# Kernel tuning notes

Measured on AMD Instinct MI355X. Metric: run time of the kernel, lower is better.

## Reference

```python
import jax, jax.numpy as jnp
import numpy as np

N_LABELS = 2048
N_CLASSES = 2
BATCH = 2048
BRANCH = 4


def _tree():
    # deterministic rooted tree: parent(i) = (i-1)//BRANCH, node 0 is root
    parent = np.full(N_LABELS, -1, dtype=np.int64)
    parent[1:] = (np.arange(1, N_LABELS) - 1) // BRANCH
    depth = np.zeros(N_LABELS, dtype=np.int64)
    for i in range(1, N_LABELS):
        depth[i] = depth[parent[i]] + 1
    levels = [np.where(depth == d)[0] for d in range(int(depth.max()) + 1)]
    return parent, levels

_PARENT, _LEVELS = _tree()  # static structure (from the adjacency init arg)


def setup_inputs() -> dict:
    key = jax.random.key(0)
    k1, k2 = jax.random.split(key)
    emissions = jax.random.normal(k1, (BATCH, N_CLASSES, N_LABELS), dtype=jnp.float32)
    pairs = jax.random.normal(k2, (N_LABELS, N_LABELS, N_CLASSES, N_CLASSES), dtype=jnp.float32)
    return {"emissions": emissions, "pairs": pairs}


def _messages(emissions, pairs, upward):
    """Belief-propagation messages, level-synchronous (topological order).

    upward=True  -> alphas: messages from children to parents (leaves->root)
    upward=False -> betas:  messages from parents to children (root->leaves)
    """
    B, C, L = emissions.shape
    acc = jnp.zeros((B, C, L), emissions.dtype)
    if upward:
        # process deepest level first; all nodes at level d send to their
        # (level d-1) parents; duplicate parent indices accumulate via .add
        for d in range(len(_LEVELS) - 1, 0, -1):
            nodes = _LEVELS[d]      # senders (children), (K,)
            par = _PARENT[nodes]    # receivers (parents), (K,)
            # local[b, k, yc] = emissions[b, yc, node_k] + acc[b, yc, node_k]
            local = (emissions[:, :, nodes] + acc[:, :, nodes]).transpose(0, 2, 1)
            trans = pairs[par, nodes]  # (K, Cp, Cc): pairs[parent, child]
            # msg[b, k, yp] = logsumexp_yc( trans[k, yp, yc] + local[b, k, yc] )
            msg = jax.nn.logsumexp(trans[None] + local[:, :, None, :], axis=-1)
            acc = acc.at[:, :, par].add(msg.transpose(0, 2, 1))
    else:
        # process shallow -> deep; each node receives from its parent,
        # whose betas were completed in the previous level iteration
        for d in range(1, len(_LEVELS)):
            nodes = _LEVELS[d]      # receivers (children)
            par = _PARENT[nodes]    # senders (parents)
            local = (emissions[:, :, par] + acc[:, :, par]).transpose(0, 2, 1)  # (B,K,Cp)
            trans = pairs[nodes, par]  # (K, Cc, Cp): pairs[child, parent]
            msg = jax.nn.logsumexp(trans[None] + local[:, :, None, :], axis=-1)  # (B,K,Cc)
            acc = acc.at[:, :, nodes].add(msg.transpose(0, 2, 1))
    return acc


def reference(emissions, pairs):
    alphas = _messages(emissions, pairs, True)
    betas = _messages(emissions, pairs, False)
    scores = emissions + alphas + betas  # (B, C, L)
    # normalize over classes per label -> log marginals log p(y_i | X)
    return scores - jax.nn.logsumexp(scores, axis=1, keepdims=True)
```

## Files before the change

### kernel.cpp

```cpp
#include <hip/hip_runtime.h>


constexpr int NLAB = 2048;
constexpr int NBATCH = 2048;

#define LOG2E 1.4426950408889634f
#define LN2   0.6931471805599453f

__device__ __forceinline__ float fexp2(float x) { return __builtin_amdgcn_exp2f(x); }
__device__ __forceinline__ float flog2(float x) { return __builtin_amdgcn_logf(x); }

__global__ __launch_bounds__(256) void compact_pairs(
    const float4* __restrict__ pairs4,
    float4* __restrict__ up,
    float4* __restrict__ down)
{
    int i = blockIdx.x * 256 + threadIdx.x;
    if (i < NLAB - 1) {
        int c = i + 1, p = i >> 2;
        float4 t = pairs4[(size_t)p * NLAB + c];
        up[i] = make_float4(t.x, t.z,
                            fexp2((t.y - t.x) * LOG2E),
                            fexp2((t.w - t.z) * LOG2E));
        float4 s = pairs4[(size_t)c * NLAB + p];
        down[i] = make_float4(s.x, s.z,
                              fexp2((s.y - s.x) * LOG2E),
                              fexp2((s.w - s.z) * LOG2E));
    }
}

__global__ __launch_bounds__(64, 2) void treecrf_kernel(
    const float* __restrict__ em_g,
    const float4* __restrict__ up,
    const float4* __restrict__ down,
    float* __restrict__ out)
{
    __shared__ float em[2 * NLAB];
    __shared__ float al[2 * 512];

    const int b = blockIdx.x;
    const int lane = threadIdx.x;
    const float4* __restrict__ eg4 =
        reinterpret_cast<const float4*>(em_g + (size_t)b * 2 * NLAB);
    float4* em4 = reinterpret_cast<float4*>(em);
    const float2* em2 = reinterpret_cast<const float2*>(em);
    float2* al2 = reinterpret_cast<float2*>(al);

#pragma unroll
    for (int k = 0; k < 8; ++k) {
        int j = k * 64 + lane;
        float4 a0 = eg4[j];
        float4 a1 = eg4[512 + j];
        em4[2 * j]     = make_float4(a0.x, a1.x, a0.y, a1.y);
        em4[2 * j + 1] = make_float4(a0.z, a1.z, a0.w, a1.w);
    }

    const int ustart[6] = {1364, 340, 84, 20, 4, 0};
    const int ucnt[6]   = {684, 1024, 256, 64, 16, 4};
#pragma unroll
    for (int pass = 0; pass < 6; ++pass) {
        const int s = ustart[pass];
        const int iters = (ucnt[pass] + 63) >> 6;
#pragma unroll
        for (int k = 0; k < iters; ++k) {
            const int i = s + k * 64 + lane;
            const bool active = (i - s) < ucnt[pass];
            const bool valid = active && (i + 1) < NLAB;
            const int c = min(i + 1, NLAB - 1);
            float2 e = em2[c];
            float l0 = e.x, l1 = e.y;
            if (pass == 1) {
                float2 a = al2[min(c, 511)];
                if (c < 512) { l0 += a.x; l1 += a.y; }
            } else if (pass >= 2) {
                float2 a = al2[c];
                l0 += a.x; l1 += a.y;
            }
            float4 t = up[min(i, NLAB - 2)];
            float eu = fexp2((l1 - l0) * LOG2E);
            float m0 = t.x + l0 + LN2 * flog2(fmaf(eu, t.z, 1.f));
            float m1 = t.y + l0 + LN2 * flog2(fmaf(eu, t.w, 1.f));
            if (!valid) { m0 = 0.f; m1 = 0.f; }
            m0 += __shfl_xor(m0, 1, 4);  m0 += __shfl_xor(m0, 2, 4);
            m1 += __shfl_xor(m1, 1, 4);  m1 += __shfl_xor(m1, 2, 4);
            if (active && (i & 3) == 0)
                al2[i >> 2] = make_float2(m0, m1);
        }
    }

    float* __restrict__ ob0 = out + (size_t)b * 2 * NLAB;
    float* __restrict__ ob1 = ob0 + NLAB;

    if (lane == 0) {
        float2 e = em2[0];
        float s0 = e.x + al[0];
        float s1 = e.y + al[1];
        float Z = s0 + LN2 * flog2(1.f + fexp2((s1 - s0) * LOG2E));
        ob0[0] = s0 - Z;
        ob1[0] = s1 - Z;
        al2[0] = make_float2(e.x, e.y);
    }

    const int dstart[6] = {1, 5, 21, 85, 341, 1365};
    const int dcnt[6]   = {4, 16, 64, 256, 1024, 683};
#pragma unroll
    for (int pass = 0; pass < 6; ++pass) {
        const int s = dstart[pass];
        const int iters = (dcnt[pass] + 63) >> 6;
#pragma unroll
        for (int k = 0; k < iters; ++k) {
            const int n = s + k * 64 + lane;
            const bool active = (n - s) < dcnt[pass];
            const int nc = active ? n : s;
            const int par = (nc - 1) >> 2;
            float2 pp = al2[par];
            float4 t = down[nc - 1];
            float eu = fexp2((pp.y - pp.x) * LOG2E);
            float m0 = t.x + pp.x + LN2 * flog2(fmaf(eu, t.z, 1.f));
            float m1 = t.y + pp.x + LN2 * flog2(fmaf(eu, t.w, 1.f));
            float2 e = em2[nc];
            float pb0 = e.x + m0;
            float pb1 = e.y + m1;
            float a0 = 0.f, a1 = 0.f;
            if (pass <= 3) {
                float2 a = al2[nc];
                a0 = a.x; a1 = a.y;
                if (active) al2[nc] = make_float2(pb0, pb1);
            } else if (pass == 4) {
                float2 a = al2[min(nc, 511)];
                if (nc < 512) {
                    a0 = a.x; a1 = a.y;
                    if (active) al2[nc] = make_float2(pb0, pb1);
                }
            }
            float s0 = pb0 + a0;
            float s1 = pb1 + a1;
            float Z = s0 + LN2 * flog2(1.f + fexp2((s1 - s0) * LOG2E));
            if (active) {
                ob0[n] = s0 - Z;
                ob1[n] = s1 - Z;
            }
        }
    }
}

extern "C" void kernel_launch(void* const* d_in, const int* in_sizes, int n_in,
                              void* d_out, int out_size, void* d_ws, size_t ws_size,
                              hipStream_t stream) {
    const float*  emissions = (const float*)d_in[0];
    const float4* pairs4    = (const float4*)d_in[1];
    float* outp             = (float*)d_out;

    float4* upw = (float4*)d_ws;
    float4* dnw = upw + (NLAB - 1);
    compact_pairs<<<dim3((NLAB + 255) / 256), dim3(256), 0, stream>>>(pairs4, upw, dnw);
    treecrf_kernel<<<dim3(NBATCH), dim3(64), 0, stream>>>(emissions, upw, dnw, outp);
}
```

Baseline: 138.1 us.

## Split each batch tree across four wavefronts by root subtree

Each block now runs four wavefronts instead of one. Each wavefront owns one of the root's four child subtrees and runs the upward and downward passes for that subtree independently. Block-wide barriers appear only around the root combine. The aim is to shorten each block's serial per-level chain and raise latency hiding, at the cost of more block-wide synchronisation and uneven work, since the wave holding the leaf tail does more. Wave-to-subtree assignment is rotated by block index to spread that imbalance across SIMDs.

Result: faster. 130.5 us (-5.5%).

```diff
diff --git a/kernel.cpp b/kernel.cpp
--- a/kernel.cpp
+++ b/kernel.cpp
@@ -29,7 +29,56 @@
     }
 }
 
-__global__ __launch_bounds__(64, 2) void treecrf_kernel(
+template <int AMODE>
+__device__ __forceinline__ float2 up_step(int i, bool active,
+        const float2* em2, float2* al2, const float4* __restrict__ upt) {
+    const bool valid = active && (i + 1) < NLAB;
+    const int c = min(i + 1, NLAB - 1);
+    float2 e = em2[c];
+    float l0 = e.x, l1 = e.y;
+    if (AMODE == 2) { float2 a = al2[c]; l0 += a.x; l1 += a.y; }
+    if (AMODE == 1) { float2 a = al2[min(c, 511)];
+                      if (c < 512) { l0 += a.x; l1 += a.y; } }
+    float4 t = upt[min(i, NLAB - 2)];
+    float eu = fexp2((l1 - l0) * LOG2E);
+    float m0 = t.x + l0 + LN2 * flog2(fmaf(eu, t.z, 1.f));
+    float m1 = t.y + l0 + LN2 * flog2(fmaf(eu, t.w, 1.f));
+    if (!valid) { m0 = 0.f; m1 = 0.f; }
+    m0 += __shfl_xor(m0, 1, 4);  m0 += __shfl_xor(m0, 2, 4);
+    m1 += __shfl_xor(m1, 1, 4);  m1 += __shfl_xor(m1, 2, 4);
+    if (active && (i & 3) == 0) al2[i >> 2] = make_float2(m0, m1);
+    return make_float2(m0, m1);
+}
+
+template <int DMODE>
+__device__ __forceinline__ void down_step(int n, bool active,
+        const float2* em2, float2* al2, const float4* __restrict__ dnt,
+        float* __restrict__ ob0, float* __restrict__ ob1) {
+    const int nc = min(n, NLAB - 1);
+    const int par = (nc - 1) >> 2;
+    float2 pp = al2[par];
+    float4 t = dnt[nc - 1];
+    float eu = fexp2((pp.y - pp.x) * LOG2E);
+    float m0 = t.x + pp.x + LN2 * flog2(fmaf(eu, t.z, 1.f));
+    float m1 = t.y + pp.x + LN2 * flog2(fmaf(eu, t.w, 1.f));
+    float2 e = em2[nc];
+    float pb0 = e.x + m0, pb1 = e.y + m1;
+    float a0 = 0.f, a1 = 0.f;
+    if (DMODE == 2) {
+        float2 a = al2[nc]; a0 = a.x; a1 = a.y;
+        if (active) al2[nc] = make_float2(pb0, pb1);
+    }
+    if (DMODE == 1) {
+        float2 a = al2[min(nc, 511)];
+        if (nc < 512) { a0 = a.x; a1 = a.y; }
+        if (active && nc < 512) al2[nc] = make_float2(pb0, pb1);
+    }
+    float s0 = pb0 + a0, s1 = pb1 + a1;
+    float Z = s0 + LN2 * flog2(1.f + fexp2((s1 - s0) * LOG2E));
+    if (active) { ob0[n] = s0 - Z; ob1[n] = s1 - Z; }
+}
+
+__global__ __launch_bounds__(256, 4) void treecrf_kernel(
     const float* __restrict__ em_g,
     const float4* __restrict__ up,
     const float4* __restrict__ down,
@@ -39,7 +88,11 @@
     __shared__ float al[2 * 512];
 
     const int b = blockIdx.x;
-    const int lane = threadIdx.x;
+    const int tid = threadIdx.x;
+    const int lane = tid & 63;
+    const int w = tid >> 6;
+    const int k = (w + b) & 3;
+
     const float4* __restrict__ eg4 =
         reinterpret_cast<const float4*>(em_g + (size_t)b * 2 * NLAB);
     float4* em4 = reinterpret_cast<float4*>(em);
@@ -47,100 +100,92 @@
     float2* al2 = reinterpret_cast<float2*>(al);
 
 #pragma unroll
-    for (int k = 0; k < 8; ++k) {
-        int j = k * 64 + lane;
+    for (int it = 0; it < 2; ++it) {
+        int j = it * 256 + tid;
         float4 a0 = eg4[j];
         float4 a1 = eg4[512 + j];
         em4[2 * j]     = make_float4(a0.x, a1.x, a0.y, a1.y);
         em4[2 * j + 1] = make_float4(a0.z, a1.z, a0.w, a1.w);
     }
-
-    const int ustart[6] = {1364, 340, 84, 20, 4, 0};
-    const int ucnt[6]   = {684, 1024, 256, 64, 16, 4};
-#pragma unroll
-    for (int pass = 0; pass < 6; ++pass) {
-        const int s = ustart[pass];
-        const int iters = (ucnt[pass] + 63) >> 6;
-#pragma unroll
-        for (int k = 0; k < iters; ++k) {
-            const int i = s + k * 64 + lane;
-            const bool active = (i - s) < ucnt[pass];
-            const bool valid = active && (i + 1) < NLAB;
-            const int c = min(i + 1, NLAB - 1);
-            float2 e = em2[c];
-            float l0 = e.x, l1 = e.y;
-            if (pass == 1) {
-                float2 a = al2[min(c, 511)];
-                if (c < 512) { l0 += a.x; l1 += a.y; }
-            } else if (pass >= 2) {
-                float2 a = al2[c];
-                l0 += a.x; l1 += a.y;
-            }
-            float4 t = up[min(i, NLAB - 2)];
-            float eu = fexp2((l1 - l0) * LOG2E);
-            float m0 = t.x + l0 + LN2 * flog2(fmaf(eu, t.z, 1.f));
-            float m1 = t.y + l0 + LN2 * flog2(fmaf(eu, t.w, 1.f));
-            if (!valid) { m0 = 0.f; m1 = 0.f; }
-            m0 += __shfl_xor(m0, 1, 4);  m0 += __shfl_xor(m0, 2, 4);
-            m1 += __shfl_xor(m1, 1, 4);  m1 += __shfl_xor(m1, 2, 4);
-            if (active && (i & 3) == 0)
-                al2[i >> 2] = make_float2(m0, m1);
+    __syncthreads();
+
+    if (k == 0) {
+#pragma unroll 4
+        for (int it = 0; it < 11; ++it) {
+            int i = 1364 + it * 64 + lane;
+            up_step<0>(i, i < 2048, em2, al2, up);
         }
-    }
+#pragma unroll
+        for (int it = 0; it < 4; ++it)
+            up_step<1>(340 + it * 64 + lane, true, em2, al2, up);
+    } else {
+        const int ib = 340 + 256 * k;
+#pragma unroll
+        for (int it = 0; it < 4; ++it)
+            up_step<0>(ib + it * 64 + lane, true, em2, al2, up);
+    }
+    up_step<2>(84 + 64 * k + lane, true, em2, al2, up);
+    up_step<2>(20 + 16 * k + lane, lane < 16, em2, al2, up);
+    float2 acc = up_step<2>(4 + 4 * k + lane, lane < 4, em2, al2, up);
+    const float alpha0 = acc.x, alpha1 = acc.y;
+
+    if (lane == 0) {
+        float2 e = em2[1 + k];
+        float l0 = e.x + alpha0, l1 = e.y + alpha1;
+        float4 t = up[k];
+        float eu = fexp2((l1 - l0) * LOG2E);
+        float m0 = t.x + l0 + LN2 * flog2(fmaf(eu, t.z, 1.f));
+        float m1 = t.y + l0 + LN2 * flog2(fmaf(eu, t.w, 1.f));
+        al2[1 + k] = make_float2(m0, m1);
+    }
+    __syncthreads();
 
     float* __restrict__ ob0 = out + (size_t)b * 2 * NLAB;
     float* __restrict__ ob1 = ob0 + NLAB;
 
+    if (tid == 0) {
+        float2 q1 = al2[1], q2 = al2[2], q3 = al2[3], q4 = al2[4];
+        float ra0 = (q1.x + q2.x) + (q3.x + q4.x);
+        float ra1 = (q1.y + q2.y) + (q3.y + q4.y);
+        float2 e = em2[0];
+        float s0 = e.x + ra0, s1 = e.y + ra1;
+        float Z = s0 + LN2 * flog2(1.f + fexp2((s1 - s0) * LOG2E));
+        ob0[0] = s0 - Z;  ob1[0] = s1 - Z;
+        al2[0] = make_float2(e.x, e.y);
+    }
+    __syncthreads();
+
     if (lane == 0) {
-        float2 e = em2[0];
-        float s0 = e.x + al[0];
-        float s1 = e.y + al[1];
+        const int n = 1 + k;
+        float2 pp = al2[0];
+        float4 t = down[k];
+        float eu = fexp2((pp.y - pp.x) * LOG2E);
+        float m0 = t.x + pp.x + LN2 * flog2(fmaf(eu, t.z, 1.f));
+        float m1 = t.y + pp.x + LN2 * flog2(fmaf(eu, t.w, 1.f));
+        float2 e = em2[n];
+        float pb0 = e.x + m0, pb1 = e.y + m1;
+        al2[n] = make_float2(pb0, pb1);
+        float s0 = pb0 + alpha0, s1 = pb1 + alpha1;
         float Z = s0 + LN2 * flog2(1.f + fexp2((s1 - s0) * LOG2E));
-        ob0[0] = s0 - Z;
-        ob1[0] = s1 - Z;
-        al2[0] = make_float2(e.x, e.y);
-    }
-
-    const int dstart[6] = {1, 5, 21, 85, 341, 1365};
-    const int dcnt[6]   = {4, 16, 64, 256, 1024, 683};
-#pragma unroll
-    for (int pass = 0; pass < 6; ++pass) {
-        const int s = dstart[pass];
-        const int iters = (dcnt[pass] + 63) >> 6;
-#pragma unroll
-        for (int k = 0; k < iters; ++k) {
-            const int n = s + k * 64 + lane;
-            const bool active = (n - s) < dcnt[pass];
-            const int nc = active ? n : s;
-            const int par = (nc - 1) >> 2;
-            float2 pp = al2[par];
-            float4 t = down[nc - 1];
-            float eu = fexp2((pp.y - pp.x) * LOG2E);
-            float m0 = t.x + pp.x + LN2 * flog2(fmaf(eu, t.z, 1.f));
-            float m1 = t.y + pp.x + LN2 * flog2(fmaf(eu, t.w, 1.f));
-            float2 e = em2[nc];
-            float pb0 = e.x + m0;
-            float pb1 = e.y + m1;
-            float a0 = 0.f, a1 = 0.f;
-            if (pass <= 3) {
-                float2 a = al2[nc];
-                a0 = a.x; a1 = a.y;
-                if (active) al2[nc] = make_float2(pb0, pb1);
-            } else if (pass == 4) {
-                float2 a = al2[min(nc, 511)];
-                if (nc < 512) {
-                    a0 = a.x; a1 = a.y;
-                    if (active) al2[nc] = make_float2(pb0, pb1);
-                }
-            }
-            float s0 = pb0 + a0;
-            float s1 = pb1 + a1;
-            float Z = s0 + LN2 * flog2(1.f + fexp2((s1 - s0) * LOG2E));
-            if (active) {
-                ob0[n] = s0 - Z;
-                ob1[n] = s1 - Z;
-            }
+        ob0[n] = s0 - Z;  ob1[n] = s1 - Z;
+    }
+    down_step<2>(5 + 4 * k + lane, lane < 4, em2, al2, down, ob0, ob1);
+    down_step<2>(21 + 16 * k + lane, lane < 16, em2, al2, down, ob0, ob1);
+    down_step<2>(85 + 64 * k + lane, true, em2, al2, down, ob0, ob1);
+    if (k == 0) {
+#pragma unroll
+        for (int it = 0; it < 4; ++it)
+            down_step<1>(341 + it * 64 + lane, true, em2, al2, down, ob0, ob1);
+#pragma unroll 4
+        for (int it = 0; it < 11; ++it) {
+            int n = 1365 + it * 64 + lane;
+            down_step<0>(n, n < 2048, em2, al2, down, ob0, ob1);
         }
+    } else {
+        const int nb = 341 + 256 * k;
+#pragma unroll
+        for (int it = 0; it < 4; ++it)
+            down_step<0>(nb + it * 64 + lane, true, em2, al2, down, ob0, ob1);
     }
 }
 
@@ -154,5 +199,5 @@
     float4* upw = (float4*)d_ws;
     float4* dnw = upw + (NLAB - 1);
     compact_pairs<<<dim3((NLAB + 255) / 256), dim3(256), 0, stream>>>(pairs4, upw, dnw);
-    treecrf_kernel<<<dim3(NBATCH), dim3(64), 0, stream>>>(emissions, upw, dnw, outp);
-}
+    treecrf_kernel<<<dim3(NBATCH), dim3(256), 0, stream>>>(emissions, upw, dnw, outp);
+}
```
